# Performance work log

Measured on AMD Instinct MI355X. Metric: run time of the kernel, lower is better.

Reference implementation:

```python
import jax, jax.numpy as jnp
import numpy as np

H = 16        # num_attention_heads
D = 1024      # hidden_size
HD = D // H   # attention_head_size = 64

def setup_inputs() -> dict:
    key = jax.random.key(0)
    ks = jax.random.split(key, 5)
    scale = 0.02
    return {
        "hidden_states": jax.random.normal(ks[0], (4, 2048, D), dtype=jnp.float32),
        "attention_mask": jnp.zeros((4, 2048), dtype=jnp.float32),
        "Wq": jax.random.normal(ks[1], (D, D), dtype=jnp.float32) * scale,
        "bq": jnp.zeros((D,), dtype=jnp.float32),
        "Wk": jax.random.normal(ks[2], (D, D), dtype=jnp.float32) * scale,
        "bk": jnp.zeros((D,), dtype=jnp.float32),
        "Wv": jax.random.normal(ks[3], (D, D), dtype=jnp.float32) * scale,
        "bv": jnp.zeros((D,), dtype=jnp.float32),
    }

def _heads(x, B, S):
    # [B,S,D] -> [B,H,S,HD]
    return x.reshape(B, S, H, HD).transpose(0, 2, 1, 3)

def reference(hidden_states, attention_mask, Wq, bq, Wk, bk, Wv, bv):
    B, S, _ = hidden_states.shape
    q = _heads(hidden_states @ Wq + bq, B, S)
    k = _heads(hidden_states @ Wk + bk, B, S)
    v = _heads(hidden_states @ Wv + bv, B, S)
    # scores: [B,H,S,S]
    scores = jnp.einsum('bhqd,bhkd->bhqk', q, k) / jnp.sqrt(jnp.float32(HD))
    scores = scores + attention_mask[:, None, None, :]  # additive mask
    probs = jax.nn.softmax(scores, axis=-1)
    # dropout is identity in eval mode
    ctx = jnp.einsum('bhqk,bhkd->bhqd', probs, v)
    return ctx.transpose(0, 2, 1, 3).reshape(B, S, H * HD)
```

## Files before the change

### kernel.cpp

```cpp
#include <hip/hip_runtime.h>


typedef __bf16 bf16_t;
typedef __bf16 bf16x2 __attribute__((ext_vector_type(2)));
typedef __bf16 bf16x4 __attribute__((ext_vector_type(4)));
typedef __bf16 bf16x8 __attribute__((ext_vector_type(8)));
typedef float floatx16 __attribute__((ext_vector_type(16)));
typedef float floatx4 __attribute__((ext_vector_type(4)));

__device__ __forceinline__ void glds16(const void* g, void* l) {
  __builtin_amdgcn_global_load_lds(
      (const __attribute__((address_space(1))) void*)g,
      (__attribute__((address_space(3))) void*)l, 16, 0, 0);
}

__device__ __forceinline__ float exp2_fast(float x) {
  return __builtin_amdgcn_exp2f(x);
}

__device__ __forceinline__ unsigned pk2(float a, float b) {
  union { bf16x2 v; unsigned u; } cv;
  cv.v[0] = (bf16_t)a; cv.v[1] = (bf16_t)b;
  return cv.u;
}

__device__ __forceinline__ void plane32(unsigned& a, unsigned& b) {
  asm("v_permlane32_swap_b32 %0, %1" : "+v"(a), "+v"(b));
}

__global__ __launch_bounds__(256) void k_prep(const float* __restrict__ X,
                                              bf16_t* __restrict__ Xb,
                                              const float* __restrict__ Wq,
                                              const float* __restrict__ Wk,
                                              const float* __restrict__ Wv,
                                              bf16_t* __restrict__ Wt) {
  int bid = blockIdx.x;
  if (bid < 8192) {
    int i = (bid * 256 + threadIdx.x) * 4;
    float4 v = *(const float4*)(X + i);
    bf16x4 o;
    o[0] = (bf16_t)v.x; o[1] = (bf16_t)v.y; o[2] = (bf16_t)v.z; o[3] = (bf16_t)v.w;
    *(bf16x4*)(Xb + i) = o;
  } else {
    int t = bid - 8192;
    int z = t >> 10, r2 = t & 1023;
    int bx = r2 & 31, by = r2 >> 5;
    const float* W = (z == 0) ? Wq : ((z == 1) ? Wk : Wv);
    bf16_t* dst = Wt + (size_t)z * 1048576;
    __shared__ float tt[32][33];
    int tx = threadIdx.x & 31, ty = threadIdx.x >> 5;
#pragma unroll
    for (int r = 0; r < 4; r++) {
      int k = by * 32 + ty + r * 8;
      tt[ty + r * 8][tx] = W[k * 1024 + bx * 32 + tx];
    }
    __syncthreads();
#pragma unroll
    for (int r = 0; r < 4; r++) {
      int n = bx * 32 + ty + r * 8;
      dst[(size_t)n * 1024 + by * 32 + tx] = (bf16_t)tt[tx][ty + r * 8];
    }
  }
}

__global__ __launch_bounds__(256) void k_qkv(
    const bf16_t* __restrict__ Xb, const bf16_t* __restrict__ Wt,
    const float* __restrict__ bq, const float* __restrict__ bk,
    const float* __restrict__ bv, bf16_t* __restrict__ Qb,
    bf16_t* __restrict__ Kb, bf16_t* __restrict__ Vt) {
  __shared__ bf16_t tA[128 * 64];
  __shared__ bf16_t tB[128 * 64];
  int tid = threadIdx.x, wv = tid >> 6, lane = tid & 63;
  int quad = lane >> 4, l16 = lane & 15;
  int wm = wv >> 1, wn = wv & 1;

  int id = blockIdx.x;
  int x = id & 7, w = id >> 3;
  int bn = w >> 3, pm = w & 7;
  int bm = x * 8 + pm;
  size_t m0 = (size_t)bm * 128, n0 = (size_t)bn * 128;
  int wsel = bn >> 3;

  floatx4 acc[4][4];
#pragma unroll
  for (int a = 0; a < 4; a++)
#pragma unroll
    for (int b = 0; b < 4; b++)
#pragma unroll
      for (int r = 0; r < 4; r++) acc[a][b][r] = 0.f;

  const bf16_t* Ab = Xb + m0 * 1024;
  const bf16_t* Bb = Wt + n0 * 1024;
  const bf16_t* fA = (wsel == 2) ? tB : tA;
  const bf16_t* fB = (wsel == 2) ? tA : tB;

  for (int k0 = 0; k0 < 1024; k0 += 64) {
    __syncthreads();
#pragma unroll
    for (int i = 0; i < 4; i++) {
      int j = wv * 4 + i;
      int row = j * 8 + (lane >> 3);
      int dblk = (lane & 7) ^ (row & 7);
      glds16(Ab + (size_t)row * 1024 + k0 + dblk * 8, tA + j * 512);
      glds16(Bb + (size_t)row * 1024 + k0 + dblk * 8, tB + j * 512);
    }
    __syncthreads();
#pragma unroll
    for (int s = 0; s < 2; s++) {
      bf16x8 av[4], bw[4];
#pragma unroll
      for (int rt = 0; rt < 4; rt++) {
        int rowa = wm * 64 + rt * 16 + l16;
        av[rt] = *(const bf16x8*)(fA + rowa * 64 + (((4 * s + quad) ^ (rowa & 7)) * 8));
        int rowb = wn * 64 + rt * 16 + l16;
        bw[rt] = *(const bf16x8*)(fB + rowb * 64 + (((4 * s + quad) ^ (rowb & 7)) * 8));
      }
#pragma unroll
      for (int rt = 0; rt < 4; rt++)
#pragma unroll
        for (int ct = 0; ct < 4; ct++)
          acc[rt][ct] = __builtin_amdgcn_mfma_f32_16x16x32_bf16(av[rt], bw[ct],
                                                               acc[rt][ct], 0, 0, 0);
    }
  }

  if (wsel == 2) {
    int bb = (int)(m0 >> 11);
#pragma unroll
    for (int rt = 0; rt < 4; rt++) {
#pragma unroll
      for (int r = 0; r < 4; r++) {
        int nl = wm * 64 + rt * 16 + quad * 4 + r;
        int n1 = ((int)n0 + nl) & 1023;
        int hh = n1 >> 6, dd = n1 & 63;
        float bi = bv[n1];
        size_t base = (size_t)(bb * 16 + hh) * 131072 + (size_t)dd * 2048;
#pragma unroll
        for (int ct = 0; ct < 4; ct++) {
          int m = (int)m0 + wn * 64 + ct * 16 + l16;
          Vt[base + (m & 2047)] = (bf16_t)(acc[rt][ct][r] + bi);
        }
      }
    }
  } else {
    const float* bias = (wsel == 0) ? bq : bk;
#pragma unroll
    for (int ct = 0; ct < 4; ct++) {
      int n = (int)n0 + wn * 64 + ct * 16 + l16;
      int n1 = n & 1023;
      int hh = n1 >> 6, dd = n1 & 63;
      float bi = bias[n1];
#pragma unroll
      for (int rt = 0; rt < 4; rt++) {
#pragma unroll
        for (int r = 0; r < 4; r++) {
          int m = (int)m0 + wm * 64 + rt * 16 + quad * 4 + r;
          int bb = m >> 11, ss = m & 2047;
          size_t bh = (size_t)(bb * 16 + hh);
          float v = acc[rt][ct][r] + bi;
          if (wsel == 0) {
            Qb[bh * 131072 + (size_t)ss * 64 + dd] = (bf16_t)(v * 0.18033688011117f);
          } else {
            Kb[bh * 131072 + (size_t)ss * 64 + dd] = (bf16_t)v;
          }
        }
      }
    }
  }
}

__global__ __launch_bounds__(256, 2) void k_attn(const bf16_t* __restrict__ Qb,
                                                 const bf16_t* __restrict__ Kb,
                                                 const bf16_t* __restrict__ VtG,
                                                 const float* __restrict__ mask,
                                                 float* __restrict__ out) {
  __shared__ float smem[10240];
  bf16_t* lds = (bf16_t*)smem;
  float* mlds = smem + 8192;

  int tid = threadIdx.x, wq = tid >> 6, lane = tid & 63;
  int q5 = lane & 31, h5 = lane >> 5;

  int id = blockIdx.x;
  int x = id & 7, w = id >> 3;
  int bh = x * 8 + (w >> 3), qt = w & 7;
  int b = bh >> 4, hh = bh & 15;

  const bf16_t* Qp = Qb + (size_t)bh * 131072;
  const bf16_t* Kp = Kb + (size_t)bh * 131072;
  const bf16_t* Vp = VtG + (size_t)bh * 131072;
  const float* mp = mask + b * 2048;

#pragma unroll
  for (int j = 0; j < 2; j++) {
    float4 mv = *(const float4*)(mp + tid * 8 + j * 4);
    float4 sv;
    sv.x = mv.x * 1.4426950408890f - 12.0f;
    sv.y = mv.y * 1.4426950408890f - 12.0f;
    sv.z = mv.z * 1.4426950408890f - 12.0f;
    sv.w = mv.w * 1.4426950408890f - 12.0f;
    *(float4*)(mlds + tid * 8 + j * 4) = sv;
  }

  int q0 = qt * 256 + wq * 64;
  bf16x8 qf0[4], qf1[4];
#pragma unroll
  for (int s = 0; s < 4; s++) {
    qf0[s] = *(const bf16x8*)(Qp + (size_t)(q0 + q5) * 64 + s * 16 + h5 * 8);
    qf1[s] = *(const bf16x8*)(Qp + (size_t)(q0 + 32 + q5) * 64 + s * 16 + h5 * 8);
  }

  union { uint4 u; bf16x8 v; } qfe;
  qfe.u.x = h5 ? 0u : 0x00003f80u;
  qfe.u.y = 0u; qfe.u.z = 0u; qfe.u.w = 0u;

  int off[2][4];
#pragma unroll
  for (int j = 0; j < 2; j++)
#pragma unroll
    for (int s = 0; s < 4; s++)
      off[j][s] = (j * 32 + q5) * 64 + (((2 * s + h5) ^ (q5 & 7)) * 8);

  int r0 = wq * 16 + (lane >> 3);
  int slot = (lane & 7) ^ ((lane >> 3) & 7);
  const bf16_t* kg0 = Kp + (size_t)r0 * 64 + slot * 8;
  const bf16_t* kg1 = kg0 + 512;
  const bf16_t* vg0 = Vp + (size_t)r0 * 2048 + slot * 8;
  const bf16_t* vg1 = vg0 + 16384;
  int c0 = wq * 2;

  floatx16 zed;
#pragma unroll
  for (int r = 0; r < 16; r++) zed[r] = 0.f;

  floatx16 ov[4];
#pragma unroll
  for (int t2 = 0; t2 < 4; t2++)
#pragma unroll
    for (int r = 0; r < 16; r++) ov[t2][r] = 0.f;
  float pa0 = 0.f, pa1 = 0.f, pa2 = 0.f, pa3 = 0.f;
  float pb0 = 0.f, pb1 = 0.f, pb2 = 0.f, pb3 = 0.f;

  {
    bf16_t* bK = lds;
    bf16_t* bV = lds + 4096;
    glds16(kg0, bK + c0 * 512); glds16(kg1, bK + c0 * 512 + 512);
    glds16(vg0, bV + c0 * 512); glds16(vg1, bV + c0 * 512 + 512);
    kg0 += 4096; kg1 += 4096; vg0 += 64; vg1 += 64;
  }

  for (int it = 0; it < 32; ++it) {
    int kk0 = it * 64, cur = it & 1;
    __syncthreads();
    if (it + 1 < 32) {
      bf16_t* bK = lds + (cur ^ 1) * 8192;
      bf16_t* bV = bK + 4096;
      glds16(kg0, bK + c0 * 512); glds16(kg1, bK + c0 * 512 + 512);
      glds16(vg0, bV + c0 * 512); glds16(vg1, bV + c0 * 512 + 512);
      kg0 += 4096; kg1 += 4096; vg0 += 64; vg1 += 64;
    }
    const bf16_t* bK = lds + cur * 8192;
    const bf16_t* bV = bK + 4096;

    union { uint4 u; bf16x8 v; } kfe[2];
    kfe[0].u.x = h5 ? 0u : pk2(mlds[kk0 + q5], 0.f);
    kfe[1].u.x = h5 ? 0u : pk2(mlds[kk0 + 32 + q5], 0.f);
    kfe[0].u.y = 0u; kfe[0].u.z = 0u; kfe[0].u.w = 0u;
    kfe[1].u.y = 0u; kfe[1].u.z = 0u; kfe[1].u.w = 0u;

#pragma unroll
    for (int tt = 0; tt < 2; tt++) {
      floatx16 a0, a1;
      __builtin_amdgcn_s_setprio(1);
      {
        bf16x8 kf = *(const bf16x8*)(bK + off[tt][0]);
        a0 = __builtin_amdgcn_mfma_f32_32x32x16_bf16(kf, qf0[0], zed, 0, 0, 0);
        a1 = __builtin_amdgcn_mfma_f32_32x32x16_bf16(kf, qf1[0], zed, 0, 0, 0);
      }
#pragma unroll
      for (int s = 1; s < 4; s++) {
        bf16x8 kf = *(const bf16x8*)(bK + off[tt][s]);
        a0 = __builtin_amdgcn_mfma_f32_32x32x16_bf16(kf, qf0[s], a0, 0, 0, 0);
        a1 = __builtin_amdgcn_mfma_f32_32x32x16_bf16(kf, qf1[s], a1, 0, 0, 0);
      }
      a0 = __builtin_amdgcn_mfma_f32_32x32x16_bf16(kfe[tt].v, qfe.v, a0, 0, 0, 0);
      a1 = __builtin_amdgcn_mfma_f32_32x32x16_bf16(kfe[tt].v, qfe.v, a1, 0, 0, 0);
      __builtin_amdgcn_s_setprio(0);

#pragma unroll
      for (int sl = 0; sl < 2; sl++) {
        int s = tt * 2 + sl, base = sl * 8;
        float e0 = exp2_fast(a0[base + 0]);
        float e1 = exp2_fast(a0[base + 1]);
        float e2 = exp2_fast(a0[base + 2]);
        float e3 = exp2_fast(a0[base + 3]);
        float e4 = exp2_fast(a0[base + 4]);
        float e5 = exp2_fast(a0[base + 5]);
        float e6 = exp2_fast(a0[base + 6]);
        float e7 = exp2_fast(a0[base + 7]);
        pa0 += e0 + e4; pa1 += e1 + e5; pa2 += e2 + e6; pa3 += e3 + e7;
        unsigned A0 = pk2(e0, e1), B0 = pk2(e2, e3);
        unsigned C0 = pk2(e4, e5), D0 = pk2(e6, e7);
        float f0 = exp2_fast(a1[base + 0]);
        float f1 = exp2_fast(a1[base + 1]);
        float f2 = exp2_fast(a1[base + 2]);
        float f3 = exp2_fast(a1[base + 3]);
        float f4 = exp2_fast(a1[base + 4]);
        float f5 = exp2_fast(a1[base + 5]);
        float f6 = exp2_fast(a1[base + 6]);
        float f7 = exp2_fast(a1[base + 7]);
        pb0 += f0 + f4; pb1 += f1 + f5; pb2 += f2 + f6; pb3 += f3 + f7;
        unsigned A1 = pk2(f0, f1), B1 = pk2(f2, f3);
        unsigned C1 = pk2(f4, f5), D1 = pk2(f6, f7);
        unsigned px0 = A0, pz0 = C0; plane32(px0, pz0);
        unsigned py0 = B0, pw0 = D0; plane32(py0, pw0);
        unsigned px1 = A1, pz1 = C1; plane32(px1, pz1);
        unsigned py1 = B1, pw1 = D1; plane32(py1, pw1);
        union { uint4 u; bf16x8 v; } pf0, pf1;
        pf0.u.x = px0; pf0.u.y = py0; pf0.u.z = pz0; pf0.u.w = pw0;
        pf1.u.x = px1; pf1.u.y = py1; pf1.u.z = pz1; pf1.u.w = pw1;
        __builtin_amdgcn_s_setprio(1);
#pragma unroll
        for (int t2 = 0; t2 < 2; t2++) {
          bf16x8 vf = *(const bf16x8*)(bV + off[t2][s]);
          ov[t2]     = __builtin_amdgcn_mfma_f32_32x32x16_bf16(vf, pf0.v, ov[t2], 0, 0, 0);
          ov[2 + t2] = __builtin_amdgcn_mfma_f32_32x32x16_bf16(vf, pf1.v, ov[2 + t2], 0, 0, 0);
        }
        __builtin_amdgcn_s_setprio(0);
      }
    }
  }

  float ls0 = (pa0 + pa1) + (pa2 + pa3);
  float ls1 = (pb0 + pb1) + (pb2 + pb3);
  ls0 += __shfl_xor(ls0, 32);
  ls1 += __shfl_xor(ls1, 32);
  float rl0 = 1.f / ls0, rl1 = 1.f / ls1;

  int qbase0 = b * 2048 + qt * 256;
#pragma unroll
  for (int half = 0; half < 2; half++) {
    __syncthreads();
    if ((wq >> 1) == half) {
      int qw = (wq & 1) * 64;
#pragma unroll
      for (int u = 0; u < 2; u++) {
        float rl = u ? rl1 : rl0;
#pragma unroll
        for (int t2 = 0; t2 < 2; t2++)
#pragma unroll
          for (int r = 0; r < 16; r++) {
            int d = t2 * 32 + (r & 3) + 8 * (r >> 2) + 4 * h5;
            smem[(qw + u * 32 + q5) * 68 + d] = ov[u * 2 + t2][r] * rl;
          }
      }
    }
    __syncthreads();
    int qbase = qbase0 + half * 128;
#pragma unroll
    for (int i = 0; i < 8; i++) {
      int slot2 = i * 256 + tid;
      int q = slot2 >> 4, c = slot2 & 15;
      float4 v = *(const float4*)(smem + q * 68 + c * 4);
      *(float4*)(out + (size_t)(qbase + q) * 1024 + hh * 64 + c * 4) = v;
    }
  }
}

extern "C" void kernel_launch(void* const* d_in, const int* in_sizes, int n_in,
                              void* d_out, int out_size, void* d_ws, size_t ws_size,
                              hipStream_t stream) {
  const float* X    = (const float*)d_in[0];
  const float* mask = (const float*)d_in[1];
  const float* Wq   = (const float*)d_in[2];
  const float* bq   = (const float*)d_in[3];
  const float* Wk   = (const float*)d_in[4];
  const float* bk   = (const float*)d_in[5];
  const float* Wv   = (const float*)d_in[6];
  const float* bv   = (const float*)d_in[7];
  float* out = (float*)d_out;

  char* ws = (char*)d_ws;
  bf16_t* Xb = (bf16_t*)ws;
  bf16_t* Wt = (bf16_t*)(ws + 16777216);
  bf16_t* Qb = (bf16_t*)(ws + 23068672);
  bf16_t* Kb = (bf16_t*)(ws + 39845888);
  bf16_t* Vt = (bf16_t*)(ws + 56623104);

  k_prep<<<11264, 256, 0, stream>>>(X, Xb, Wq, Wk, Wv, Wt);
  k_qkv<<<1536, 256, 0, stream>>>(Xb, Wt, bq, bk, bv, Qb, Kb, Vt);
  k_attn<<<512, 256, 0, stream>>>(Qb, Kb, Vt, mask, out);
}
```

Before: 237.8 us.

## Stage QKV epilogue through LDS for coalesced stores; hoist K/V fragment loads

The QKV projection epilogue now writes bias-added bf16 results into shared memory, then stores them to global with 16-byte vectorized, contiguous writes for Q, K and transposed V. This replaces the previous scattered 2-byte stores, which were badly uncoalesced for the V transpose. In the attention kernel, all K and V fragment LDS reads for a sub-tile are issued before the MFMA chain, and the row-sum accumulators use packed float2 adds. These add LDS traffic, extra barriers and register pressure in exchange for better global store efficiency and latency hiding.

```diff
diff --git a/kernel.cpp b/kernel.cpp
--- a/kernel.cpp
+++ b/kernel.cpp
@@ -7,6 +7,7 @@
 typedef __bf16 bf16x8 __attribute__((ext_vector_type(8)));
 typedef float floatx16 __attribute__((ext_vector_type(16)));
 typedef float floatx4 __attribute__((ext_vector_type(4)));
+typedef float floatx2 __attribute__((ext_vector_type(2)));
 
 __device__ __forceinline__ void glds16(const void* g, void* l) {
   __builtin_amdgcn_global_load_lds(
@@ -68,8 +69,9 @@
     const float* __restrict__ bq, const float* __restrict__ bk,
     const float* __restrict__ bv, bf16_t* __restrict__ Qb,
     bf16_t* __restrict__ Kb, bf16_t* __restrict__ Vt) {
-  __shared__ bf16_t tA[128 * 64];
-  __shared__ bf16_t tB[128 * 64];
+  __shared__ bf16_t shmem[16384];
+  bf16_t* tA = shmem;
+  bf16_t* tB = shmem + 8192;
   int tid = threadIdx.x, wv = tid >> 6, lane = tid & 63;
   int quad = lane >> 4, l16 = lane & 15;
   int wm = wv >> 1, wn = wv & 1;
@@ -124,47 +126,62 @@
     }
   }
 
+  __syncthreads();
+  int s0 = (int)(m0 & 2047), bb = (int)(m0 >> 11);
+  int hbase = ((int)(n0 & 1023)) >> 6;
+
   if (wsel == 2) {
-    int bb = (int)(m0 >> 11);
 #pragma unroll
     for (int rt = 0; rt < 4; rt++) {
 #pragma unroll
       for (int r = 0; r < 4; r++) {
         int nl = wm * 64 + rt * 16 + quad * 4 + r;
         int n1 = ((int)n0 + nl) & 1023;
-        int hh = n1 >> 6, dd = n1 & 63;
         float bi = bv[n1];
-        size_t base = (size_t)(bb * 16 + hh) * 131072 + (size_t)dd * 2048;
 #pragma unroll
         for (int ct = 0; ct < 4; ct++) {
-          int m = (int)m0 + wn * 64 + ct * 16 + l16;
-          Vt[base + (m & 2047)] = (bf16_t)(acc[rt][ct][r] + bi);
+          int ml = wn * 64 + ct * 16 + l16;
+          shmem[nl * 128 + ml] = (bf16_t)(acc[rt][ct][r] + bi);
         }
       }
+    }
+    __syncthreads();
+#pragma unroll
+    for (int p = 0; p < 8; p++) {
+      int c = p * 256 + tid;
+      int nl = c >> 4, mo = (c & 15) * 8;
+      bf16x8 vv = *(const bf16x8*)(shmem + nl * 128 + mo);
+      int hh = hbase + (nl >> 6), dd = nl & 63;
+      *(bf16x8*)(Vt + (size_t)(bb * 16 + hh) * 131072 + (size_t)dd * 2048 + s0 + mo) = vv;
     }
   } else {
     const float* bias = (wsel == 0) ? bq : bk;
 #pragma unroll
     for (int ct = 0; ct < 4; ct++) {
-      int n = (int)n0 + wn * 64 + ct * 16 + l16;
-      int n1 = n & 1023;
-      int hh = n1 >> 6, dd = n1 & 63;
+      int n1 = ((int)n0 + wn * 64 + ct * 16 + l16) & 1023;
       float bi = bias[n1];
 #pragma unroll
       for (int rt = 0; rt < 4; rt++) {
 #pragma unroll
         for (int r = 0; r < 4; r++) {
-          int m = (int)m0 + wm * 64 + rt * 16 + quad * 4 + r;
-          int bb = m >> 11, ss = m & 2047;
-          size_t bh = (size_t)(bb * 16 + hh);
+          int ml = wm * 64 + rt * 16 + quad * 4 + r;
+          int nl = wn * 64 + ct * 16 + l16;
           float v = acc[rt][ct][r] + bi;
-          if (wsel == 0) {
-            Qb[bh * 131072 + (size_t)ss * 64 + dd] = (bf16_t)(v * 0.18033688011117f);
-          } else {
-            Kb[bh * 131072 + (size_t)ss * 64 + dd] = (bf16_t)v;
-          }
+          shmem[ml * 128 + nl] =
+              (wsel == 0) ? (bf16_t)(v * 0.18033688011117f) : (bf16_t)v;
         }
       }
+    }
+    __syncthreads();
+    bf16_t* outp = (wsel == 0) ? Qb : Kb;
+#pragma unroll
+    for (int p = 0; p < 8; p++) {
+      int c = p * 256 + tid;
+      int h = c >> 10, c1 = c & 1023;
+      int ml = c1 >> 3, ko = (c1 & 7) * 8;
+      bf16x8 vv = *(const bf16x8*)(shmem + ml * 128 + h * 64 + ko);
+      *(bf16x8*)(outp + (size_t)(bb * 16 + hbase + h) * 131072 +
+                 (size_t)(s0 + ml) * 64 + ko) = vv;
     }
   }
 }
@@ -238,8 +255,9 @@
   for (int t2 = 0; t2 < 4; t2++)
 #pragma unroll
     for (int r = 0; r < 16; r++) ov[t2][r] = 0.f;
-  float pa0 = 0.f, pa1 = 0.f, pa2 = 0.f, pa3 = 0.f;
-  float pb0 = 0.f, pb1 = 0.f, pb2 = 0.f, pb3 = 0.f;
+  floatx2 pA0, pA1, pB0, pB1;
+  pA0[0] = pA0[1] = pA1[0] = pA1[1] = 0.f;
+  pB0[0] = pB0[1] = pB1[0] = pB1[1] = 0.f;
 
   {
     bf16_t* bK = lds;
@@ -270,18 +288,23 @@
 
 #pragma unroll
     for (int tt = 0; tt < 2; tt++) {
+      bf16x8 kf[4], vfa[2], vfb[2];
+#pragma unroll
+      for (int s = 0; s < 4; s++) kf[s] = *(const bf16x8*)(bK + off[tt][s]);
+#pragma unroll
+      for (int t2 = 0; t2 < 2; t2++) {
+        vfa[t2] = *(const bf16x8*)(bV + off[t2][tt * 2]);
+        vfb[t2] = *(const bf16x8*)(bV + off[t2][tt * 2 + 1]);
+      }
+
       floatx16 a0, a1;
       __builtin_amdgcn_s_setprio(1);
-      {
-        bf16x8 kf = *(const bf16x8*)(bK + off[tt][0]);
-        a0 = __builtin_amdgcn_mfma_f32_32x32x16_bf16(kf, qf0[0], zed, 0, 0, 0);
-        a1 = __builtin_amdgcn_mfma_f32_32x32x16_bf16(kf, qf1[0], zed, 0, 0, 0);
-      }
+      a0 = __builtin_amdgcn_mfma_f32_32x32x16_bf16(kf[0], qf0[0], zed, 0, 0, 0);
+      a1 = __builtin_amdgcn_mfma_f32_32x32x16_bf16(kf[0], qf1[0], zed, 0, 0, 0);
 #pragma unroll
       for (int s = 1; s < 4; s++) {
-        bf16x8 kf = *(const bf16x8*)(bK + off[tt][s]);
-        a0 = __builtin_amdgcn_mfma_f32_32x32x16_bf16(kf, qf0[s], a0, 0, 0, 0);
-        a1 = __builtin_amdgcn_mfma_f32_32x32x16_bf16(kf, qf1[s], a1, 0, 0, 0);
+        a0 = __builtin_amdgcn_mfma_f32_32x32x16_bf16(kf[s], qf0[s], a0, 0, 0, 0);
+        a1 = __builtin_amdgcn_mfma_f32_32x32x16_bf16(kf[s], qf1[s], a1, 0, 0, 0);
       }
       a0 = __builtin_amdgcn_mfma_f32_32x32x16_bf16(kfe[tt].v, qfe.v, a0, 0, 0, 0);
       a1 = __builtin_amdgcn_mfma_f32_32x32x16_bf16(kfe[tt].v, qfe.v, a1, 0, 0, 0);
@@ -289,7 +312,7 @@
 
 #pragma unroll
       for (int sl = 0; sl < 2; sl++) {
-        int s = tt * 2 + sl, base = sl * 8;
+        int base = sl * 8;
         float e0 = exp2_fast(a0[base + 0]);
         float e1 = exp2_fast(a0[base + 1]);
         float e2 = exp2_fast(a0[base + 2]);
@@ -298,7 +321,9 @@
         float e5 = exp2_fast(a0[base + 5]);
         float e6 = exp2_fast(a0[base + 6]);
         float e7 = exp2_fast(a0[base + 7]);
-        pa0 += e0 + e4; pa1 += e1 + e5; pa2 += e2 + e6; pa3 += e3 + e7;
+        floatx2 u0, u1;
+        u0[0] = e0 + e4; u0[1] = e1 + e5; pA0 += u0;
+        u1[0] = e2 + e6; u1[1] = e3 + e7; pA1 += u1;
         unsigned A0 = pk2(e0, e1), B0 = pk2(e2, e3);
         unsigned C0 = pk2(e4, e5), D0 = pk2(e6, e7);
         float f0 = exp2_fast(a1[base + 0]);
@@ -309,7 +334,9 @@
         float f5 = exp2_fast(a1[base + 5]);
         float f6 = exp2_fast(a1[base + 6]);
         float f7 = exp2_fast(a1[base + 7]);
-        pb0 += f0 + f4; pb1 += f1 + f5; pb2 += f2 + f6; pb3 += f3 + f7;
+        floatx2 w0, w1;
+        w0[0] = f0 + f4; w0[1] = f1 + f5; pB0 += w0;
+        w1[0] = f2 + f6; w1[1] = f3 + f7; pB1 += w1;
         unsigned A1 = pk2(f0, f1), B1 = pk2(f2, f3);
         unsigned C1 = pk2(f4, f5), D1 = pk2(f6, f7);
         unsigned px0 = A0, pz0 = C0; plane32(px0, pz0);
@@ -322,7 +349,7 @@
         __builtin_amdgcn_s_setprio(1);
 #pragma unroll
         for (int t2 = 0; t2 < 2; t2++) {
-          bf16x8 vf = *(const bf16x8*)(bV + off[t2][s]);
+          bf16x8 vf = sl ? vfb[t2] : vfa[t2];
           ov[t2]     = __builtin_amdgcn_mfma_f32_32x32x16_bf16(vf, pf0.v, ov[t2], 0, 0, 0);
           ov[2 + t2] = __builtin_amdgcn_mfma_f32_32x32x16_bf16(vf, pf1.v, ov[2 + t2], 0, 0, 0);
         }
@@ -331,8 +358,8 @@
     }
   }
 
-  float ls0 = (pa0 + pa1) + (pa2 + pa3);
-  float ls1 = (pb0 + pb1) + (pb2 + pb3);
+  float ls0 = (pA0[0] + pA0[1]) + (pA1[0] + pA1[1]);
+  float ls1 = (pB0[0] + pB0[1]) + (pB1[0] + pB1[1]);
   ls0 += __shfl_xor(ls0, 32);
   ls1 += __shfl_xor(ls1, 32);
   float rl0 = 1.f / ls0, rl1 = 1.f / ls1;
```

New measurement: 236.4 us. Within noise of the previous version (-0.6%).
